# Optimization experiments

Hardware: AMD Instinct MI355X
Metric: run time of the kernel (lower is better)

The kernel has to match this reference:

```python
import jax, jax.numpy as jnp
import numpy as np

N_NODES = 100000
N_EDGES = 1600000
D = 128
L = 3


def setup_inputs() -> dict:
    key = jax.random.key(0)
    k1, k2, k3 = jax.random.split(key, 3)
    edge_index = jax.random.randint(k1, (2, N_EDGES), 0, N_NODES, dtype=jnp.int64)
    emb = jax.random.normal(k2, (N_NODES, D), dtype=jnp.float32)
    # Glorot-style scale for the per-layer linear weights
    Ws = jax.random.normal(k3, (L, D, D), dtype=jnp.float32) * (1.0 / np.sqrt(D))
    bs = jnp.zeros((L, D), dtype=jnp.float32)
    return {"edge_index": edge_index, "emb": emb, "Ws": Ws, "bs": bs}


def _gcn_forward(emb, Ws, bs, edge_index):
    n = emb.shape[0]
    self_loop = jnp.arange(n, dtype=edge_index.dtype)
    # PyG GCNConv adds self-loops and uses symmetric normalization
    row = jnp.concatenate([edge_index[0], self_loop])  # source nodes
    col = jnp.concatenate([edge_index[1], self_loop])  # target nodes
    deg = jax.ops.segment_sum(jnp.ones(row.shape[0], dtype=emb.dtype), col, num_segments=n)
    deg_inv_sqrt = jnp.where(deg > 0, jax.lax.rsqrt(jnp.maximum(deg, 1.0)), 0.0)
    norm = deg_inv_sqrt[row] * deg_inv_sqrt[col]  # [E+N]

    x = emb
    for l in range(Ws.shape[0]):
        h = x @ Ws[l]                              # [N, D] linear transform
        msg = h[row] * norm[:, None]               # gather + scale [E+N, D]
        x = jax.ops.segment_sum(msg, col, num_segments=n) + bs[l]  # scatter-add
        x = jax.nn.relu(x)                         # dropout is identity in eval
    return x


def reference(edge_index, emb, Ws, bs) -> jnp.ndarray:
    return _gcn_forward(emb, Ws, bs, edge_index)
```

## Files before the change

kernel.cpp:

```cpp
#include <hip/hip_runtime.h>
#include <hip/hip_fp16.h>
#include <cstdint>
#include <cstddef>

#define N_NODES 100000
#define N_EDGES 1600000
#define D 128
#define NLAYERS 3
#define NB 3125
#define NBLK_E 128
#define EPB 12500
#define ENT_CAP 1024

typedef float f2v __attribute__((ext_vector_type(2)));
typedef _Float16 f16x8 __attribute__((ext_vector_type(8)));
typedef float f32x4 __attribute__((ext_vector_type(4)));
typedef unsigned u32x4 __attribute__((ext_vector_type(4)));


__global__ __launch_bounds__(512) void hist1_kernel(const int* __restrict__ col,
                                                    int* __restrict__ hmat) {
    __shared__ int hist[NB];
    int b = blockIdx.x, t = threadIdx.x;
    for (int j = t; j < NB; j += 512) hist[j] = 0;
    __syncthreads();
    int base = b * EPB;
    for (int i = t; i < EPB; i += 512) {
        int c = col[base + i];
        atomicAdd(&hist[c >> 5], 1);
    }
    __syncthreads();
    for (int j = t; j < NB; j += 512) hmat[b * NB + j] = hist[j];
}

__global__ void btot_kernel(const int* __restrict__ hmat, int* __restrict__ btot) {
    int j = blockIdx.x * 256 + threadIdx.x;
    if (j < NB) {
        int s = 0;
        for (int b = 0; b < NBLK_E; b++) s += hmat[b * NB + j];
        btot[j] = s;
    }
}

__global__ void bscan_kernel(const int* __restrict__ btot, int* __restrict__ bstart, int nb, int e) {
    __shared__ int lsum[1024];
    int t = threadIdx.x;
    int vals[4];
    int v0 = 0;
#pragma unroll
    for (int j = 0; j < 4; j++) {
        int idx = t * 4 + j;
        int c = (idx < nb) ? btot[idx] : 0;
        vals[j] = c;
        v0 += c;
    }
    lsum[t] = v0;
    __syncthreads();
    for (int off = 1; off < 1024; off <<= 1) {
        int x = (t >= off) ? lsum[t - off] : 0;
        __syncthreads();
        lsum[t] += x;
        __syncthreads();
    }
    int base = lsum[t] - v0;
#pragma unroll
    for (int j = 0; j < 4; j++) {
        int idx = t * 4 + j;
        if (idx < nb) {
            bstart[idx] = base;
            base += vals[j];
        }
    }
    if (t == 0) bstart[nb] = e;
}

__global__ void hoff_kernel(const int* __restrict__ hmat, const int* __restrict__ bstart,
                            int* __restrict__ hoff) {
    int j = blockIdx.x * 256 + threadIdx.x;
    if (j < NB) {
        int run = bstart[j];
        for (int b = 0; b < NBLK_E; b++) {
            hoff[b * NB + j] = run;
            run += hmat[b * NB + j];
        }
    }
}

__global__ __launch_bounds__(512) void scatter_kernel(const int* __restrict__ row,
                                                      const int* __restrict__ col,
                                                      const int* __restrict__ hoff,
                                                      unsigned* __restrict__ bucketbuf) {
    __shared__ int cur[NB];
    int b = blockIdx.x, t = threadIdx.x;
    for (int j = t; j < NB; j += 512) cur[j] = hoff[b * NB + j];
    __syncthreads();
    int base = b * EPB;
    for (int i = t; i < EPB; i += 512) {
        int r = row[base + i], c = col[base + i];
        int pos = atomicAdd(&cur[c >> 5], 1);
        bucketbuf[pos] = ((unsigned)r << 5) | (unsigned)(c & 31);
    }
}

__global__ void fill2_kernel(const unsigned* __restrict__ bucketbuf, const int* __restrict__ bstart,
                             int* __restrict__ offsets, float* __restrict__ dinv,
                             int* __restrict__ src, int n, int e) {
    __shared__ unsigned ent[ENT_CAP];
    __shared__ int hist[32];
    __shared__ int cur[32];
    __shared__ int loff[32];
    int b = blockIdx.x, t = threadIdx.x;
    int s0 = bstart[b];
    int cnt = bstart[b + 1] - s0;
    if (cnt > ENT_CAP) cnt = ENT_CAP;
    if (t < 32) hist[t] = 0;
    __syncthreads();
    for (int i = t; i < cnt; i += 256) {
        unsigned v = bucketbuf[s0 + i];
        ent[i] = v;
        atomicAdd(&hist[v & 31], 1);
    }
    __syncthreads();
    if (t == 0) {
        int run = s0;
#pragma unroll
        for (int j = 0; j < 32; j++) {
            loff[j] = run;
            run += hist[j];
        }
    }
    __syncthreads();
    if (t < 32) {
        int node = b * 32 + t;
        int o = loff[t];
        offsets[node] = o;
        cur[t] = o;
        dinv[node] = rsqrtf((float)(hist[t] + 1));
    }
    if (b == 0 && t == 0) offsets[n] = e;
    __syncthreads();
    for (int i = t; i < cnt; i += 256) {
        unsigned v = ent[i];
        int pos = atomicAdd(&cur[v & 31], 1);
        src[pos] = (int)(v >> 5);
    }
}


__global__ void cast_kernel(const float2* __restrict__ in, const float* __restrict__ dinv,
                            __half2* __restrict__ out, int n2) {
    int i = blockIdx.x * 256 + threadIdx.x;
    if (i < n2) {
        float d = dinv[i >> 6];
        float2 v = in[i];
        out[i] = __floats2half2_rn(d * v.x, d * v.y);
    }
}

__global__ void wsplit_kernel(const float* __restrict__ W,
                              _Float16* __restrict__ Wh, _Float16* __restrict__ Wl) {
    int c = blockIdx.x, l = blockIdx.y, k = threadIdx.x;
    float w = W[(size_t)l * 16384 + k * 128 + c];
    _Float16 h = (_Float16)w;
    float r = w - (float)h;
    Wh[(size_t)l * 16384 + c * 128 + k] = h;
    Wl[(size_t)l * 16384 + c * 128 + k] = (_Float16)r;
}

__global__ void agg_kernel(const __half2* __restrict__ xs, const int* __restrict__ offs,
                           unsigned* __restrict__ Ah,
                           const float* __restrict__ dinv, const int* __restrict__ src,
                           int vbase) {
    int v = vbase + blockIdx.x;
    int f = threadIdx.x;
    float dv = dinv[v];
    float2 a0 = __half22float2(xs[(size_t)v * 64 + f]);
    float ax = a0.x;
    float ay = a0.y;
    int i = offs[v], s1 = offs[v + 1];
    for (; i + 7 < s1; i += 8) {
        int s[8];
#pragma unroll
        for (int j = 0; j < 8; j++) s[j] = src[i + j];
        float2 x[8];
#pragma unroll
        for (int j = 0; j < 8; j++) x[j] = __half22float2(xs[(size_t)s[j] * 64 + f]);
#pragma unroll
        for (int j = 0; j < 8; j++) {
            ax += x[j].x;
            ay += x[j].y;
        }
    }
    if (i < s1) {
        int last = s1 - 1;
        int s[8];
        float m[8];
#pragma unroll
        for (int j = 0; j < 8; j++) {
            int idx = i + j;
            bool in = idx < s1;
            s[j] = src[in ? idx : last];
            m[j] = in ? 1.0f : 0.0f;
        }
        float2 x[8];
#pragma unroll
        for (int j = 0; j < 8; j++) x[j] = __half22float2(xs[(size_t)s[j] * 64 + f]);
#pragma unroll
        for (int j = 0; j < 8; j++) {
            ax += m[j] * x[j].x;
            ay += m[j] * x[j].y;
        }
    }
    float rx = dv * ax, ry = dv * ay;
    __half2 h2 = __floats2half2_rn(rx, ry);
    Ah[(size_t)v * 64 + f] = __builtin_bit_cast(unsigned, h2);
}

__global__ __launch_bounds__(256, 6) void gemm_mfma_kernel(
    const _Float16* __restrict__ Ahp,
    const _Float16* __restrict__ Whp, const _Float16* __restrict__ Wlp,
    const float* __restrict__ bias, float* __restrict__ out,
    __half2* __restrict__ xs_out, const float* __restrict__ dinv,
    int write_h, int write_out) {
    __shared__ _Float16 sA[32][136];
    int t = threadIdx.x;
    int f = t & 63;
    int w = t >> 6;
    int row0 = blockIdx.x * 32;

    const u32x4* Aq = (const u32x4*)Ahp;
#pragma unroll
    for (int i = 0; i < 2; i++) {
        int qid = t + 256 * i;
        int r = qid >> 4;
        int k2 = qid & 15;
        u32x4 v = Aq[(size_t)(row0 + r) * 16 + k2];
        *(u32x4*)&sA[r][k2 * 8] = v;
    }
    __syncthreads();

    int lrow = f & 15, kg = f >> 4;
    f32x4 acc[2][2];
#pragma unroll
    for (int m = 0; m < 2; m++)
#pragma unroll
        for (int c = 0; c < 2; c++) acc[m][c] = (f32x4){0.f, 0.f, 0.f, 0.f};

#pragma unroll
    for (int ks = 0; ks < 4; ks++) {
        int g = ks * 4 + kg;
        f16x8 a0 = *(const f16x8*)&sA[lrow][g * 8];
        f16x8 a1 = *(const f16x8*)&sA[16 + lrow][g * 8];
#pragma unroll
        for (int c = 0; c < 2; c++) {
            int col = w * 32 + c * 16 + lrow;
            f16x8 bh = *(const f16x8*)&Whp[(size_t)col * 128 + g * 8];
            f16x8 bl = *(const f16x8*)&Wlp[(size_t)col * 128 + g * 8];
            acc[0][c] = __builtin_amdgcn_mfma_f32_16x16x32_f16(a0, bh, acc[0][c], 0, 0, 0);
            acc[0][c] = __builtin_amdgcn_mfma_f32_16x16x32_f16(a0, bl, acc[0][c], 0, 0, 0);
            acc[1][c] = __builtin_amdgcn_mfma_f32_16x16x32_f16(a1, bh, acc[1][c], 0, 0, 0);
            acc[1][c] = __builtin_amdgcn_mfma_f32_16x16x32_f16(a1, bl, acc[1][c], 0, 0, 0);
        }
    }

    float bcol[2];
    bcol[0] = bias[w * 32 + 0 * 16 + lrow];
    bcol[1] = bias[w * 32 + 1 * 16 + lrow];
#pragma unroll
    for (int m = 0; m < 2; m++) {
        int rbase = row0 + m * 16 + kg * 4;
#pragma unroll
        for (int j = 0; j < 4; j++) {
            int rowi = rbase + j;
            float dvr = write_h ? dinv[rowi] : 0.f;
#pragma unroll
            for (int c = 0; c < 2; c++) {
                float o = fmaxf(acc[m][c][j] + bcol[c], 0.f);
                float o2 = __shfl_xor(o, 1);
                int col = w * 32 + c * 16 + lrow;
                if (write_out)
                    __builtin_nontemporal_store(o, out + (size_t)rowi * 128 + col);
                if (write_h && !(f & 1))
                    xs_out[(size_t)rowi * 64 + (col >> 1)] =
                        __floats2half2_rn(dvr * o, dvr * o2);
            }
        }
    }
}


extern "C" void kernel_launch(void* const* d_in, const int* in_sizes, int n_in,
                              void* d_out, int out_size, void* d_ws, size_t ws_size,
                              hipStream_t stream) {
    const int* edge = (const int*)d_in[0];
    const float* emb = (const float*)d_in[1];
    const float* Ws = (const float*)d_in[2];
    const float* bs = (const float*)d_in[3];
    float* out = (float*)d_out;

    const int n = N_NODES, e = N_EDGES;
    const int* row = edge;
    const int* col = edge + e;

    char* p = (char*)d_ws;
    _Float16* Ah = (_Float16*)p;
    int* hmat = (int*)p;
    int* hoff = hmat + (size_t)NBLK_E * NB;
    p += (size_t)n * D * 2;
    __half2* xs = (__half2*)p;
    unsigned* bucketbuf = (unsigned*)p;
    p += (size_t)n * D * 2;
    int* csr_src  = (int*)p;    p += (size_t)e * 4;
    float* dinv   = (float*)p;  p += (size_t)n * 4;
    int* offsets  = (int*)p;    p += (size_t)(n + 1) * 4;
    int* btot     = (int*)p;    p += (size_t)NB * 4;
    int* bstart   = (int*)p;    p += (size_t)(NB + 1) * 4;
    _Float16* WhT = (_Float16*)p; p += (size_t)NLAYERS * D * D * 2;
    _Float16* WlT = (_Float16*)p; p += (size_t)NLAYERS * D * D * 2;

    hist1_kernel<<<NBLK_E, 512, 0, stream>>>(col, hmat);
    btot_kernel<<<(NB + 255) / 256, 256, 0, stream>>>(hmat, btot);
    bscan_kernel<<<1, 1024, 0, stream>>>(btot, bstart, NB, e);
    hoff_kernel<<<(NB + 255) / 256, 256, 0, stream>>>(hmat, bstart, hoff);
    scatter_kernel<<<NBLK_E, 512, 0, stream>>>(row, col, hoff, bucketbuf);
    fill2_kernel<<<NB, 256, 0, stream>>>(bucketbuf, bstart, offsets, dinv, csr_src, n, e);
    wsplit_kernel<<<dim3(128, NLAYERS), 128, 0, stream>>>(Ws, WhT, WlT);

    int n2 = n * 64;
    cast_kernel<<<(n2 + 255) / 256, 256, 0, stream>>>((const float2*)emb, dinv, xs, n2);

    const int half = n / 2;
    for (int l = 0; l < NLAYERS; l++) {
        agg_kernel<<<half, 64, 0, stream>>>(xs, offsets, (unsigned*)Ah,
                                            dinv, csr_src, 0);
        agg_kernel<<<half, 64, 0, stream>>>(xs, offsets, (unsigned*)Ah,
                                            dinv, csr_src, half);
        gemm_mfma_kernel<<<n / 32, 256, 0, stream>>>(
            Ah, WhT + (size_t)l * D * D, WlT + (size_t)l * D * D,
            bs + (size_t)l * D, out, xs, dinv,
            (l < NLAYERS - 1) ? 1 : 0, (l == NLAYERS - 1) ? 1 : 0);
    }
}
```

Before: 477.2 us.

## Split edge histogram work across more blocks and chunk the bucket offset scan

Raises the number of edge-partition blocks for the histogram and scatter passes from 128 to 512, so the whole GPU is busy during CSR construction. The per-bucket column sums and per-block offsets are now computed in eight chunks over a 2D grid, instead of 13 blocks each walking all blocks serially. The global bucket start is added inside the scatter kernel. In exchange the histogram and offset matrices are four times larger, which means more global traffic and more per-block shared-memory init and writeback.

```diff
diff --git a/kernel.cpp b/kernel.cpp
--- a/kernel.cpp
+++ b/kernel.cpp
@@ -8,8 +8,9 @@
 #define D 128
 #define NLAYERS 3
 #define NB 3125
-#define NBLK_E 128
-#define EPB 12500
+#define NBLK_E 512
+#define EPB 3125
+#define NCHUNK 8
 #define ENT_CAP 1024
 
 typedef float f2v __attribute__((ext_vector_type(2)));
@@ -33,16 +34,20 @@
     for (int j = t; j < NB; j += 512) hmat[b * NB + j] = hist[j];
 }
 
-__global__ void btot_kernel(const int* __restrict__ hmat, int* __restrict__ btot) {
+__global__ __launch_bounds__(256) void bpart_kernel(const int* __restrict__ hmat,
+                                                    int* __restrict__ bpart) {
     int j = blockIdx.x * 256 + threadIdx.x;
+    int c = blockIdx.y;
     if (j < NB) {
         int s = 0;
-        for (int b = 0; b < NBLK_E; b++) s += hmat[b * NB + j];
-        btot[j] = s;
-    }
-}
-
-__global__ void bscan_kernel(const int* __restrict__ btot, int* __restrict__ bstart, int nb, int e) {
+        int b0 = c * 64;
+        for (int b = b0; b < b0 + 64; b++) s += hmat[(size_t)b * NB + j];
+        bpart[c * NB + j] = s;
+    }
+}
+
+__global__ void bscan_kernel(const int* __restrict__ bpart, int* __restrict__ bstart,
+                             int nb, int e) {
     __shared__ int lsum[1024];
     int t = threadIdx.x;
     int vals[4];
@@ -50,7 +55,11 @@
 #pragma unroll
     for (int j = 0; j < 4; j++) {
         int idx = t * 4 + j;
-        int c = (idx < nb) ? btot[idx] : 0;
+        int c = 0;
+        if (idx < nb) {
+#pragma unroll
+            for (int k = 0; k < NCHUNK; k++) c += bpart[k * NB + idx];
+        }
         vals[j] = c;
         v0 += c;
     }
@@ -74,14 +83,18 @@
     if (t == 0) bstart[nb] = e;
 }
 
-__global__ void hoff_kernel(const int* __restrict__ hmat, const int* __restrict__ bstart,
-                            int* __restrict__ hoff) {
+__global__ __launch_bounds__(256) void hoff2_kernel(const int* __restrict__ hmat,
+                                                    const int* __restrict__ bpart,
+                                                    int* __restrict__ hoff) {
     int j = blockIdx.x * 256 + threadIdx.x;
+    int c = blockIdx.y;
     if (j < NB) {
-        int run = bstart[j];
-        for (int b = 0; b < NBLK_E; b++) {
-            hoff[b * NB + j] = run;
-            run += hmat[b * NB + j];
+        int run = 0;
+        for (int k = 0; k < c; k++) run += bpart[k * NB + j];
+        int b0 = c * 64;
+        for (int b = b0; b < b0 + 64; b++) {
+            hoff[(size_t)b * NB + j] = run;
+            run += hmat[(size_t)b * NB + j];
         }
     }
 }
@@ -89,10 +102,12 @@
 __global__ __launch_bounds__(512) void scatter_kernel(const int* __restrict__ row,
                                                       const int* __restrict__ col,
                                                       const int* __restrict__ hoff,
+                                                      const int* __restrict__ bstart,
                                                       unsigned* __restrict__ bucketbuf) {
     __shared__ int cur[NB];
     int b = blockIdx.x, t = threadIdx.x;
-    for (int j = t; j < NB; j += 512) cur[j] = hoff[b * NB + j];
+    for (int j = t; j < NB; j += 512)
+        cur[j] = hoff[(size_t)b * NB + j] + bstart[j];
     __syncthreads();
     int base = b * EPB;
     for (int i = t; i < EPB; i += 512) {
@@ -306,6 +321,7 @@
     _Float16* Ah = (_Float16*)p;
     int* hmat = (int*)p;
     int* hoff = hmat + (size_t)NBLK_E * NB;
+    int* bpart = hoff + (size_t)NBLK_E * NB;
     p += (size_t)n * D * 2;
     __half2* xs = (__half2*)p;
     unsigned* bucketbuf = (unsigned*)p;
@@ -313,16 +329,15 @@
     int* csr_src  = (int*)p;    p += (size_t)e * 4;
     float* dinv   = (float*)p;  p += (size_t)n * 4;
     int* offsets  = (int*)p;    p += (size_t)(n + 1) * 4;
-    int* btot     = (int*)p;    p += (size_t)NB * 4;
     int* bstart   = (int*)p;    p += (size_t)(NB + 1) * 4;
     _Float16* WhT = (_Float16*)p; p += (size_t)NLAYERS * D * D * 2;
     _Float16* WlT = (_Float16*)p; p += (size_t)NLAYERS * D * D * 2;
 
     hist1_kernel<<<NBLK_E, 512, 0, stream>>>(col, hmat);
-    btot_kernel<<<(NB + 255) / 256, 256, 0, stream>>>(hmat, btot);
-    bscan_kernel<<<1, 1024, 0, stream>>>(btot, bstart, NB, e);
-    hoff_kernel<<<(NB + 255) / 256, 256, 0, stream>>>(hmat, bstart, hoff);
-    scatter_kernel<<<NBLK_E, 512, 0, stream>>>(row, col, hoff, bucketbuf);
+    bpart_kernel<<<dim3(13, NCHUNK), 256, 0, stream>>>(hmat, bpart);
+    bscan_kernel<<<1, 1024, 0, stream>>>(bpart, bstart, NB, e);
+    hoff2_kernel<<<dim3(13, NCHUNK), 256, 0, stream>>>(hmat, bpart, hoff);
+    scatter_kernel<<<NBLK_E, 512, 0, stream>>>(row, col, hoff, bstart, bucketbuf);
     fill2_kernel<<<NB, 256, 0, stream>>>(bucketbuf, bstart, offsets, dinv, csr_src, n, e);
     wsplit_kernel<<<dim3(128, NLAYERS), 128, 0, stream>>>(Ws, WhT, WlT);
 
```

New measurement: 463.4 us. -2.9%, faster.
